# Optimization experiments

Measured on AMD Instinct MI355X. Metric: run time of the kernel, lower is better.

The kernel has to match this reference:

```python
import jax, jax.numpy as jnp
import numpy as np
from jax import lax

B, S, C = 128, 512, 16
V, CV = 50000, 100
E, CE = 100, 30
H = 128        # hidden per direction (hidden_dim=256 // 2)
T = 17         # tagset size
NF = 25        # filters per char-conv
LSTM_IN = E + 3 * NF  # 175


def setup_inputs() -> dict:
    key = jax.random.key(0)
    ks = jax.random.split(key, 25)
    sc = 0.1
    inp = {
        "x": jax.random.randint(ks[0], (B, S), 0, V),
        "char_x": jax.random.randint(ks[1], (B, S, C), 0, CV),
        "tags": jax.random.randint(ks[2], (B, S), 0, T),
        "mask": jnp.ones((B, S), dtype=bool),
        "word_emb": jax.random.normal(ks[3], (V, E), jnp.float32) * sc,
        "char_emb": jax.random.normal(ks[4], (CV, CE), jnp.float32) * sc,
        "conv2_W": jax.random.normal(ks[5], (NF, CE, 2), jnp.float32) * sc,
        "conv2_b": jnp.zeros((NF,), jnp.float32),
        "conv3_W": jax.random.normal(ks[6], (NF, CE, 3), jnp.float32) * sc,
        "conv3_b": jnp.zeros((NF,), jnp.float32),
        "conv4_W": jax.random.normal(ks[7], (NF, CE, 4), jnp.float32) * sc,
        "conv4_b": jnp.zeros((NF,), jnp.float32),
        "W_ih_f": jax.random.normal(ks[8], (4 * H, LSTM_IN), jnp.float32) * sc,
        "W_hh_f": jax.random.normal(ks[9], (4 * H, H), jnp.float32) * sc,
        "b_f": jnp.zeros((4 * H,), jnp.float32),
        "W_ih_b": jax.random.normal(ks[10], (4 * H, LSTM_IN), jnp.float32) * sc,
        "W_hh_b": jax.random.normal(ks[11], (4 * H, H), jnp.float32) * sc,
        "b_b": jnp.zeros((4 * H,), jnp.float32),
        "h2t_W": jax.random.normal(ks[12], (T, 2 * H), jnp.float32) * sc,
        "h2t_b": jnp.zeros((T,), jnp.float32),
        "crf_start": jax.random.normal(ks[13], (T,), jnp.float32) * sc,
        "crf_end": jax.random.normal(ks[14], (T,), jnp.float32) * sc,
        "crf_trans": jax.random.normal(ks[15], (T, T), jnp.float32) * sc,
    }
    return inp


def _char_conv(ce, W, b):
    # ce: [BS, CE, C], W: [O, I, K] -> [BS, O] after relu + max-over-time
    out = lax.conv_general_dilated(ce, W, (1,), 'VALID',
                                   dimension_numbers=('NCH', 'OIH', 'NCH'))
    out = jax.nn.relu(out + b[None, :, None])
    return jnp.max(out, axis=-1)


def _lstm_dir(xs, W_ih, W_hh, b, reverse):
    # xs: [B, S, D] -> hs [B, S, H]; PyTorch gate order i,f,g,o
    xs_t = jnp.swapaxes(xs, 0, 1)  # [S, B, D]
    if reverse:
        xs_t = xs_t[::-1]
    pre = jnp.einsum('sbd,gd->sbg', xs_t, W_ih) + b  # hoist input projection
    h0 = jnp.zeros((xs.shape[0], H), xs.dtype)

    def step(carry, p_t):
        h, c = carry
        g = p_t + h @ W_hh.T
        i = jax.nn.sigmoid(g[:, :H])
        f = jax.nn.sigmoid(g[:, H:2 * H])
        gg = jnp.tanh(g[:, 2 * H:3 * H])
        o = jax.nn.sigmoid(g[:, 3 * H:])
        c = f * c + i * gg
        h = o * jnp.tanh(c)
        return (h, c), h

    _, hs = lax.scan(step, (h0, h0), pre)
    if reverse:
        hs = hs[::-1]
    return jnp.swapaxes(hs, 0, 1)


def _crf_nll(emissions, tags, mask, start, end, trans):
    # emissions [B,S,T]; returns sum over batch of -log p(tags | emissions)
    maskf = mask.astype(emissions.dtype)
    # ---- numerator (gold score) ----
    em_sc = jnp.take_along_axis(emissions, tags[..., None], axis=2)[..., 0]  # [B,S]
    tr_sc = trans[tags[:, :-1], tags[:, 1:]]                                  # [B,S-1]
    last_idx = jnp.sum(mask, axis=1).astype(jnp.int32) - 1
    last_tag = tags[jnp.arange(tags.shape[0]), last_idx]
    score = (start[tags[:, 0]] + em_sc[:, 0]
             + jnp.sum(maskf[:, 1:] * (tr_sc + em_sc[:, 1:]), axis=1)
             + end[last_tag])
    # ---- partition via forward-algorithm scan ----
    em_t = jnp.swapaxes(emissions, 0, 1)  # [S,B,T]
    alpha0 = start[None, :] + em_t[0]     # [B,T]

    def step(alpha, inputs):
        e_t, m_t = inputs  # [B,T], [B]
        new = jax.nn.logsumexp(alpha[:, :, None] + trans[None] + e_t[:, None, :], axis=1)
        alpha = jnp.where(m_t[:, None], new, alpha)
        return alpha, None

    alpha, _ = lax.scan(step, alpha0, (em_t[1:], jnp.swapaxes(mask, 0, 1)[1:]))
    logZ = jax.nn.logsumexp(alpha + end[None, :], axis=1)
    return jnp.sum(logZ - score)


def reference(x, char_x, tags, mask, word_emb, char_emb,
              conv2_W, conv2_b, conv3_W, conv3_b, conv4_W, conv4_b,
              W_ih_f, W_hh_f, b_f, W_ih_b, W_hh_b, b_b,
              h2t_W, h2t_b, crf_start, crf_end, crf_trans):
    # word + char features
    we = word_emb[x]                                     # [B,S,E]
    ce = char_emb[char_x].reshape(B * S, C, CE)          # [BS,C,CE]
    ce = jnp.swapaxes(ce, 1, 2)                          # [BS,CE,C]
    cf = jnp.concatenate([_char_conv(ce, conv2_W, conv2_b),
                          _char_conv(ce, conv3_W, conv3_b),
                          _char_conv(ce, conv4_W, conv4_b)], axis=1)
    cf = cf.reshape(B, S, 3 * NF)
    feats = jnp.concatenate([we, cf], axis=2)            # [B,S,175]
    # BiLSTM
    h_fwd = _lstm_dir(feats, W_ih_f, W_hh_f, b_f, reverse=False)
    h_bwd = _lstm_dir(feats, W_ih_b, W_hh_b, b_b, reverse=True)
    h = jnp.concatenate([h_fwd, h_bwd], axis=2)          # [B,S,2H]
    emissions = jnp.einsum('bsh,th->bst', h, h2t_W) + h2t_b
    # CRF NLL (model returns -crf(...), torchcrf reduction='sum')
    return _crf_nll(emissions, tags, mask, crf_start, crf_end, crf_trans)
```

## Files before the change

kernel.cpp:

```cpp
#include <hip/hip_runtime.h>
#include <hip/hip_bf16.h>

#define B_ 128
#define S_ 512
#define C_ 16
#define E_ 100
#define CE_ 30
#define NF_ 25
#define H_ 128
#define T_ 17
#define LSTM_IN_ 175
#define G4_ 512

typedef __hip_bfloat16 bf16;

__device__ __forceinline__ float bf2f(unsigned short u){
  union { unsigned int i; float f; } v; v.i = ((unsigned int)u) << 16; return v.f;
}
__device__ __forceinline__ float sigm_f(float x){
  float e = __expf(-x);
  return __builtin_amdgcn_rcpf(1.0f + e);
}
__device__ __forceinline__ float tanh_f(float x){
  x = fminf(15.0f, fmaxf(-15.0f, x));
  float e = __expf(-2.0f*x);
  return (1.0f - e) * __builtin_amdgcn_rcpf(1.0f + e);
}

__global__ __launch_bounds__(256) void word_emb_kernel(const int* __restrict__ x,
    const float* __restrict__ wemb, bf16* __restrict__ feats){
  int word = blockIdx.x*2 + (threadIdx.x>>7);
  int e = threadIdx.x & 127;
  if (e < E_) feats[(size_t)word*LSTM_IN_ + e] = __float2bfloat16(wemb[(size_t)x[word]*E_ + e]);
}

template<int KW>
__global__ __launch_bounds__(256) void char_conv_kernel(const int* __restrict__ char_x,
    const float* __restrict__ cemb, const float* __restrict__ W,
    const float* __restrict__ bias, bf16* __restrict__ feats, int out_off){
  int task = blockIdx.x*256 + threadIdx.x;
  int word = task / NF_;
  int fi = task - word*NF_;
  const int* cx = char_x + word*C_;
  float w[KW*CE_];
  #pragma unroll
  for (int i=0;i<KW*CE_;++i) w[i] = W[fi*CE_*KW + i];
  const int NP = C_ - KW + 1;
  float acc[C_ - KW + 1];
  #pragma unroll
  for (int p=0;p<NP;++p) acc[p] = 0.0f;
  #pragma unroll
  for (int c=0;c<C_;++c){
    int ci = cx[c];
    const float* ce = cemb + ci*CE_;
    #pragma unroll
    for (int e=0;e<CE_;++e){
      float v = ce[e];
      #pragma unroll
      for (int dx=0;dx<KW;++dx){
        int p = c - dx;
        if (p >= 0 && p < NP) acc[p] = fmaf(v, w[e*KW+dx], acc[p]);
      }
    }
  }
  float m = acc[0];
  #pragma unroll
  for (int p=1;p<NP;++p) m = fmaxf(m, acc[p]);
  feats[(size_t)word*LSTM_IN_ + out_off + fi] = __float2bfloat16(fmaxf(0.0f, m + bias[fi]));
}

#define BM 128
#define BN 128
#define BK 32
#define LDK 36
__global__ __launch_bounds__(256) void pre_gemm_kernel(const bf16* __restrict__ feats,
    const float* __restrict__ Wf, const float* __restrict__ Wb,
    const float* __restrict__ bf_, const float* __restrict__ bb_,
    bf16* __restrict__ pre){
  __shared__ float As[BM*LDK];
  __shared__ float Bs[BN*LDK];
  int br = blockIdx.x;
  int bc = blockIdx.y;
  int dir = bc >> 2;
  int g0 = (bc & 3) * BN;
  const float* W = dir ? Wb : Wf;
  const float* bias = dir ? bb_ : bf_;
  int tid = threadIdx.x;
  int tr = tid >> 4;
  int tc = tid & 15;
  float acc[8][8];
  #pragma unroll
  for (int i=0;i<8;++i)
    #pragma unroll
    for (int j=0;j<8;++j) acc[i][j] = 0.0f;
  for (int k0 = 0; k0 < LSTM_IN_; k0 += BK){
    for (int l = tid; l < BM*BK; l += 256){
      int r = l >> 5;
      int k = l & 31;
      int kk = k0 + k;
      float av = (kk < LSTM_IN_) ? __bfloat162float(feats[(size_t)(br*BM + r)*LSTM_IN_ + kk]) : 0.0f;
      float bv = (kk < LSTM_IN_) ? W[(size_t)(g0 + r)*LSTM_IN_ + kk] : 0.0f;
      As[r*LDK + k] = av;
      Bs[r*LDK + k] = bv;
    }
    __syncthreads();
    for (int k=0;k<BK;k+=4){
      float4 a4[8], b4[8];
      #pragma unroll
      for (int i=0;i<8;++i) a4[i] = *(const float4*)&As[(tr + 16*i)*LDK + k];
      #pragma unroll
      for (int j=0;j<8;++j) b4[j] = *(const float4*)&Bs[(tc + 16*j)*LDK + k];
      #pragma unroll
      for (int i=0;i<8;++i)
        #pragma unroll
        for (int j=0;j<8;++j){
          acc[i][j] = fmaf(a4[i].x, b4[j].x, acc[i][j]);
          acc[i][j] = fmaf(a4[i].y, b4[j].y, acc[i][j]);
          acc[i][j] = fmaf(a4[i].z, b4[j].z, acc[i][j]);
          acc[i][j] = fmaf(a4[i].w, b4[j].w, acc[i][j]);
        }
    }
    __syncthreads();
  }
  #pragma unroll
  for (int i=0;i<8;++i){
    int word = br*BM + tr + 16*i;
    int b = word >> 9;
    int s = word & 511;
    #pragma unroll
    for (int j=0;j<8;++j){
      int g = g0 + tc + 16*j;
      pre[(size_t)dir*33554432 + (size_t)b*262144 + (size_t)s*512 + g] =
          __float2bfloat16(acc[i][j] + bias[g]);
    }
  }
}

__global__ __launch_bounds__(512) void lstm_kernel(const bf16* __restrict__ pre,
    const float* __restrict__ Whh_f, const float* __restrict__ Whh_b,
    bf16* __restrict__ hs){
  int blk = blockIdx.x;
  int dir = blk & 1;
  int b = blk >> 1;
  int g = threadIdx.x;
  const float* Whh = dir ? Whh_b : Whh_f;
  float w[128];
  {
    const float* Wrow = Whh + g*H_;
    #pragma unroll
    for (int k4=0;k4<32;++k4){
      float4 v = *(const float4*)&Wrow[k4*4];
      w[4*k4+0]=v.x; w[4*k4+1]=v.y; w[4*k4+2]=v.z; w[4*k4+3]=v.w;
    }
  }
  __shared__ __align__(16) float h_lds[H_];
  __shared__ float gates[G4_];
  if (g < H_) h_lds[g] = 0.0f;
  __syncthreads();
  const bf16* preB = pre + ((size_t)dir*B_ + b)*S_*G4_;
  bf16* hsB = hs + ((size_t)dir*B_ + b)*S_*H_;
  float c = 0.0f;
  int sect = g >> 7;
  float nxt = __bfloat162float(preB[(size_t)(dir ? (S_-1) : 0)*G4_ + g]);
  for (int s=0;s<S_;++s){
    int idx = dir ? (S_-1-s) : s;
    float acc = nxt;
    if (s+1 < S_){
      int idx1 = dir ? (S_-2-s) : (s+1);
      nxt = __bfloat162float(preB[(size_t)idx1*G4_ + g]);
    }
    #pragma unroll
    for (int k4=0;k4<32;++k4){
      float4 h4 = *(const float4*)&h_lds[k4*4];
      acc = fmaf(w[4*k4+0], h4.x, acc);
      acc = fmaf(w[4*k4+1], h4.y, acc);
      acc = fmaf(w[4*k4+2], h4.z, acc);
      acc = fmaf(w[4*k4+3], h4.w, acc);
    }
    float a = (sect == 2) ? tanh_f(acc) : sigm_f(acc);
    gates[g] = a;
    __syncthreads();
    if (g < H_){
      float iv = gates[g];
      float fv = gates[g+128];
      float gv = gates[g+256];
      float ov = gates[g+384];
      c = fmaf(fv, c, iv*gv);
      float hn = ov * tanh_f(c);
      h_lds[g] = hn;
      hsB[(size_t)idx*H_ + g] = __float2bfloat16(hn);
    }
    __syncthreads();
  }
}

__global__ __launch_bounds__(256) void emis_kernel(const bf16* __restrict__ hs,
    const float* __restrict__ W, const float* __restrict__ bias, float* __restrict__ em){
  int task = blockIdx.x*256 + threadIdx.x;
  int word = task / T_;
  int t = task - word*T_;
  const ushort4* hf = (const ushort4*)(hs + (size_t)word*H_);
  const ushort4* hb = (const ushort4*)(hs + (size_t)(B_*S_ + word)*H_);
  const float* w0 = W + t*2*H_;
  float acc = bias[t];
  #pragma unroll
  for (int j4=0;j4<32;++j4){
    ushort4 u = hf[j4];
    float4 w4 = *(const float4*)&w0[j4*4];
    acc = fmaf(bf2f(u.x),w4.x,acc); acc = fmaf(bf2f(u.y),w4.y,acc);
    acc = fmaf(bf2f(u.z),w4.z,acc); acc = fmaf(bf2f(u.w),w4.w,acc);
  }
  #pragma unroll
  for (int j4=0;j4<32;++j4){
    ushort4 u = hb[j4];
    float4 w4 = *(const float4*)&w0[H_ + j4*4];
    acc = fmaf(bf2f(u.x),w4.x,acc); acc = fmaf(bf2f(u.y),w4.y,acc);
    acc = fmaf(bf2f(u.z),w4.z,acc); acc = fmaf(bf2f(u.w),w4.w,acc);
  }
  em[(size_t)word*T_ + t] = acc;
}

__global__ __launch_bounds__(256) void score_kernel(const int* __restrict__ tags,
    const float* __restrict__ em, const float* __restrict__ start,
    const float* __restrict__ end_, const float* __restrict__ trans,
    float* __restrict__ score){
  int b = blockIdx.x;
  int tid = threadIdx.x;
  const int* tg = tags + b*S_;
  const float* eb = em + (size_t)b*S_*T_;
  float s = 0.0f;
  for (int t = tid; t < S_; t += 256){
    int cur = tg[t];
    s += eb[(size_t)t*T_ + cur];
    if (t > 0) s += trans[tg[t-1]*T_ + cur];
  }
  if (tid == 0) s += start[tg[0]] + end_[tg[S_-1]];
  __shared__ float red[256];
  red[tid] = s; __syncthreads();
  for (int off=128; off; off>>=1){
    if (tid < off) red[tid] += red[tid+off];
    __syncthreads();
  }
  if (tid == 0) score[b] = red[0];
}

__global__ __launch_bounds__(64) void crf_alpha_kernel(const float* __restrict__ em,
    const float* __restrict__ start, const float* __restrict__ end_,
    const float* __restrict__ trans, float* __restrict__ logZ){
  int b = blockIdx.x;
  int j = threadIdx.x;
  __shared__ float al[T_];
  const float* eb = em + (size_t)b*S_*T_;
  float tcol[T_];
  if (j < T_){
    #pragma unroll
    for (int i=0;i<T_;++i) tcol[i] = trans[i*T_ + j];
    al[j] = start[j] + eb[j];
  }
  __syncthreads();
  float e_cur = (j < T_) ? eb[T_ + j] : 0.0f;
  for (int s=1;s<S_;++s){
    float e_nxt = (j < T_ && s+1 < S_) ? eb[(size_t)(s+1)*T_ + j] : 0.0f;
    float nv = 0.0f;
    if (j < T_){
      float av[T_];
      float m = -1e30f;
      #pragma unroll
      for (int i=0;i<T_;++i){ av[i] = al[i] + tcol[i]; m = fmaxf(m, av[i]); }
      float sum = 0.0f;
      #pragma unroll
      for (int i=0;i<T_;++i) sum += __expf(av[i]-m);
      nv = m + __logf(sum) + e_cur;
    }
    __syncthreads();
    if (j < T_) al[j] = nv;
    __syncthreads();
    e_cur = e_nxt;
  }
  if (j == 0){
    float m = -1e30f;
    float v[T_];
    #pragma unroll
    for (int i=0;i<T_;++i){ v[i] = al[i] + end_[i]; m = fmaxf(m, v[i]); }
    float sum = 0.0f;
    #pragma unroll
    for (int i=0;i<T_;++i) sum += __expf(v[i]-m);
    logZ[b] = m + __logf(sum);
  }
}

__global__ __launch_bounds__(128) void final_kernel(const float* __restrict__ logZ,
    const float* __restrict__ score, float* __restrict__ out){
  int tid = threadIdx.x;
  float v = logZ[tid] - score[tid];
  __shared__ float red[128];
  red[tid] = v; __syncthreads();
  for (int off=64; off; off>>=1){
    if (tid < off) red[tid] += red[tid+off];
    __syncthreads();
  }
  if (tid == 0) out[0] = red[0];
}

extern "C" void kernel_launch(void* const* d_in, const int* in_sizes, int n_in,
                              void* d_out, int out_size, void* d_ws, size_t ws_size,
                              hipStream_t stream) {
  const int*   x       = (const int*)  d_in[0];
  const int*   char_x  = (const int*)  d_in[1];
  const int*   tags    = (const int*)  d_in[2];
  const float* wemb    = (const float*)d_in[4];
  const float* cemb    = (const float*)d_in[5];
  const float* c2W     = (const float*)d_in[6];
  const float* c2b     = (const float*)d_in[7];
  const float* c3W     = (const float*)d_in[8];
  const float* c3b     = (const float*)d_in[9];
  const float* c4W     = (const float*)d_in[10];
  const float* c4b     = (const float*)d_in[11];
  const float* Wih_f   = (const float*)d_in[12];
  const float* Whh_f   = (const float*)d_in[13];
  const float* b_f     = (const float*)d_in[14];
  const float* Wih_b   = (const float*)d_in[15];
  const float* Whh_b   = (const float*)d_in[16];
  const float* b_b     = (const float*)d_in[17];
  const float* h2tW    = (const float*)d_in[18];
  const float* h2tb    = (const float*)d_in[19];
  const float* crf_s   = (const float*)d_in[20];
  const float* crf_e   = (const float*)d_in[21];
  const float* crf_t   = (const float*)d_in[22];
  float* out = (float*)d_out;

  const size_t NEEDED = 190710784ULL;
  if (ws_size < NEEDED) return;
  char* wsb = (char*)d_ws;
  bf16*  feats = (bf16*)(wsb);
  bf16*  pre   = (bf16*)(wsb + 22937600);
  bf16*  hs    = (bf16*)(wsb + 157155328);
  float* em    = (float*)(wsb);
  float* score = (float*)(wsb + 190709760);
  float* logZ  = (float*)(wsb + 190710272);

  word_emb_kernel<<<32768, 256, 0, stream>>>(x, wemb, feats);
  char_conv_kernel<2><<<6400, 256, 0, stream>>>(char_x, cemb, c2W, c2b, feats, E_);
  char_conv_kernel<3><<<6400, 256, 0, stream>>>(char_x, cemb, c3W, c3b, feats, E_ + NF_);
  char_conv_kernel<4><<<6400, 256, 0, stream>>>(char_x, cemb, c4W, c4b, feats, E_ + 2*NF_);
  pre_gemm_kernel<<<dim3(512, 8), 256, 0, stream>>>(feats, Wih_f, Wih_b, b_f, b_b, pre);
  lstm_kernel<<<256, 512, 0, stream>>>(pre, Whh_f, Whh_b, hs);
  emis_kernel<<<4352, 256, 0, stream>>>(hs, h2tW, h2tb, em);
  score_kernel<<<128, 256, 0, stream>>>(tags, em, crf_s, crf_e, crf_t, score);
  crf_alpha_kernel<<<128, 64, 0, stream>>>(em, crf_s, crf_e, crf_t, logZ);
  final_kernel<<<1, 128, 0, stream>>>(logZ, score, out);
}
```

Measured before the change: 1.854 ms.

## Use bf16 MFMA for the input-projection GEMM with K padded to 192

Replaces the scalar fp32 FMA tiled GEMM that computes LSTM input pre-activations with a bf16 MFMA 16x16x32 kernel. Feature rows are padded to 192 columns, with a zero-fill kernel for the padding, and the input weights are packed to bf16 with the same padding by a new kernel, so tiles can be loaded with 16-byte vector loads. The workspace layout is reorganised so feats and hs share a region. The cost is two extra small launches, and the weights are rounded to bf16 before the multiply, which adds precision loss.

```diff
diff --git a/kernel.cpp b/kernel.cpp
--- a/kernel.cpp
+++ b/kernel.cpp
@@ -10,9 +10,12 @@
 #define H_ 128
 #define T_ 17
 #define LSTM_IN_ 175
+#define KP_ 192
 #define G4_ 512
 
 typedef __hip_bfloat16 bf16;
+typedef short bf16x8 __attribute__((ext_vector_type(8)));
+typedef float f32x4 __attribute__((ext_vector_type(4)));
 
 __device__ __forceinline__ float bf2f(unsigned short u){
   union { unsigned int i; float f; } v; v.i = ((unsigned int)u) << 16; return v.f;
@@ -27,11 +30,18 @@
   return (1.0f - e) * __builtin_amdgcn_rcpf(1.0f + e);
 }
 
+__global__ __launch_bounds__(256) void zero_pad_kernel(bf16* __restrict__ feats){
+  int task = blockIdx.x*256 + threadIdx.x;
+  int word = task / 17;
+  int col = LSTM_IN_ + (task - word*17);
+  feats[(size_t)word*KP_ + col] = __float2bfloat16(0.0f);
+}
+
 __global__ __launch_bounds__(256) void word_emb_kernel(const int* __restrict__ x,
     const float* __restrict__ wemb, bf16* __restrict__ feats){
   int word = blockIdx.x*2 + (threadIdx.x>>7);
   int e = threadIdx.x & 127;
-  if (e < E_) feats[(size_t)word*LSTM_IN_ + e] = __float2bfloat16(wemb[(size_t)x[word]*E_ + e]);
+  if (e < E_) feats[(size_t)word*KP_ + e] = __float2bfloat16(wemb[(size_t)x[word]*E_ + e]);
 }
 
 template<int KW>
@@ -66,72 +76,86 @@
   float m = acc[0];
   #pragma unroll
   for (int p=1;p<NP;++p) m = fmaxf(m, acc[p]);
-  feats[(size_t)word*LSTM_IN_ + out_off + fi] = __float2bfloat16(fmaxf(0.0f, m + bias[fi]));
-}
-
-#define BM 128
-#define BN 128
-#define BK 32
-#define LDK 36
-__global__ __launch_bounds__(256) void pre_gemm_kernel(const bf16* __restrict__ feats,
-    const float* __restrict__ Wf, const float* __restrict__ Wb,
-    const float* __restrict__ bf_, const float* __restrict__ bb_,
-    bf16* __restrict__ pre){
-  __shared__ float As[BM*LDK];
-  __shared__ float Bs[BN*LDK];
+  feats[(size_t)word*KP_ + out_off + fi] = __float2bfloat16(fmaxf(0.0f, m + bias[fi]));
+}
+
+__global__ __launch_bounds__(192) void wpack_kernel(const float* __restrict__ Wf,
+    const float* __restrict__ Wb, bf16* __restrict__ wpk){
+  int g = blockIdx.x;
+  int k = threadIdx.x;
+  float v = 0.0f;
+  if (k < LSTM_IN_) v = (g < 512) ? Wf[g*LSTM_IN_ + k] : Wb[(g-512)*LSTM_IN_ + k];
+  wpk[(size_t)g*KP_ + k] = __float2bfloat16(v);
+}
+
+__global__ __launch_bounds__(256) void pre_gemm_mfma(const bf16* __restrict__ feats,
+    const bf16* __restrict__ wpk, const float* __restrict__ bf_,
+    const float* __restrict__ bb_, bf16* __restrict__ pre){
+  __shared__ __align__(16) short As[4096];
+  __shared__ __align__(16) short Bs[4096];
   int br = blockIdx.x;
   int bc = blockIdx.y;
   int dir = bc >> 2;
-  int g0 = (bc & 3) * BN;
-  const float* W = dir ? Wb : Wf;
+  int g0 = (bc & 3) * 128;
   const float* bias = dir ? bb_ : bf_;
   int tid = threadIdx.x;
-  int tr = tid >> 4;
-  int tc = tid & 15;
-  float acc[8][8];
-  #pragma unroll
-  for (int i=0;i<8;++i)
-    #pragma unroll
-    for (int j=0;j<8;++j) acc[i][j] = 0.0f;
-  for (int k0 = 0; k0 < LSTM_IN_; k0 += BK){
-    for (int l = tid; l < BM*BK; l += 256){
-      int r = l >> 5;
-      int k = l & 31;
-      int kk = k0 + k;
-      float av = (kk < LSTM_IN_) ? __bfloat162float(feats[(size_t)(br*BM + r)*LSTM_IN_ + kk]) : 0.0f;
-      float bv = (kk < LSTM_IN_) ? W[(size_t)(g0 + r)*LSTM_IN_ + kk] : 0.0f;
-      As[r*LDK + k] = av;
-      Bs[r*LDK + k] = bv;
-    }
-    __syncthreads();
-    for (int k=0;k<BK;k+=4){
-      float4 a4[8], b4[8];
-      #pragma unroll
-      for (int i=0;i<8;++i) a4[i] = *(const float4*)&As[(tr + 16*i)*LDK + k];
-      #pragma unroll
-      for (int j=0;j<8;++j) b4[j] = *(const float4*)&Bs[(tc + 16*j)*LDK + k];
-      #pragma unroll
-      for (int i=0;i<8;++i)
-        #pragma unroll
-        for (int j=0;j<8;++j){
-          acc[i][j] = fmaf(a4[i].x, b4[j].x, acc[i][j]);
-          acc[i][j] = fmaf(a4[i].y, b4[j].y, acc[i][j]);
-          acc[i][j] = fmaf(a4[i].z, b4[j].z, acc[i][j]);
-          acc[i][j] = fmaf(a4[i].w, b4[j].w, acc[i][j]);
-        }
-    }
-    __syncthreads();
-  }
-  #pragma unroll
-  for (int i=0;i<8;++i){
-    int word = br*BM + tr + 16*i;
-    int b = word >> 9;
-    int s = word & 511;
-    #pragma unroll
-    for (int j=0;j<8;++j){
-      int g = g0 + tc + 16*j;
-      pre[(size_t)dir*33554432 + (size_t)b*262144 + (size_t)s*512 + g] =
-          __float2bfloat16(acc[i][j] + bias[g]);
+  int wave = tid >> 6, lane = tid & 63;
+  int wr = wave >> 1, wc = wave & 1;
+  const bf16* Arow = feats + (size_t)br*128*KP_;
+  const bf16* Brow = wpk + (size_t)(dir*512 + g0)*KP_;
+  f32x4 acc[4][4];
+  #pragma unroll
+  for (int i=0;i<4;++i)
+    #pragma unroll
+    for (int j=0;j<4;++j) acc[i][j] = (f32x4){0.f,0.f,0.f,0.f};
+
+  for (int k0=0; k0<KP_; k0+=32){
+    int4 va[2], vb[2];
+    #pragma unroll
+    for (int hh=0; hh<2; ++hh){
+      int slot = tid + hh*256;
+      int l = slot & 63;
+      int row = ((slot>>6)<<4) + (l & 15);
+      int kb = l >> 4;
+      va[hh] = *(const int4*)(Arow + row*KP_ + k0 + kb*8);
+      vb[hh] = *(const int4*)(Brow + row*KP_ + k0 + kb*8);
+    }
+    __syncthreads();
+    #pragma unroll
+    for (int hh=0; hh<2; ++hh){
+      int slot = tid + hh*256;
+      *(int4*)&As[slot*8] = va[hh];
+      *(int4*)&Bs[slot*8] = vb[hh];
+    }
+    __syncthreads();
+    bf16x8 af[4], bfr[4];
+    #pragma unroll
+    for (int i=0;i<4;++i) af[i]  = *(const bf16x8*)&As[(wr*4+i)*512 + lane*8];
+    #pragma unroll
+    for (int j=0;j<4;++j) bfr[j] = *(const bf16x8*)&Bs[(wc*4+j)*512 + lane*8];
+    #pragma unroll
+    for (int i=0;i<4;++i)
+      #pragma unroll
+      for (int j=0;j<4;++j)
+        acc[i][j] = __builtin_amdgcn_mfma_f32_16x16x32_bf16(af[i], bfr[j], acc[i][j], 0, 0, 0);
+  }
+  int row_l = (lane>>4)*4;
+  int col_l = lane & 15;
+  float bias_v[4];
+  #pragma unroll
+  for (int j=0;j<4;++j) bias_v[j] = bias[g0 + wc*64 + j*16 + col_l];
+  #pragma unroll
+  for (int i=0;i<4;++i){
+    #pragma unroll
+    for (int q=0;q<4;++q){
+      int word = br*128 + wr*64 + i*16 + row_l + q;
+      int bidx = word >> 9, sidx = word & 511;
+      size_t base = ((size_t)(dir*B_ + bidx)*S_ + sidx)*G4_;
+      #pragma unroll
+      for (int j=0;j<4;++j){
+        int g = g0 + wc*64 + j*16 + col_l;
+        pre[base + g] = __float2bfloat16(acc[i][j][q] + bias_v[j]);
+      }
     }
   }
 }
@@ -329,21 +353,24 @@
   const float* crf_t   = (const float*)d_in[22];
   float* out = (float*)d_out;
 
-  const size_t NEEDED = 190710784ULL;
+  const size_t NEEDED = 167773184ULL;
   if (ws_size < NEEDED) return;
   char* wsb = (char*)d_ws;
-  bf16*  feats = (bf16*)(wsb);
-  bf16*  pre   = (bf16*)(wsb + 22937600);
-  bf16*  hs    = (bf16*)(wsb + 157155328);
+  bf16*  pre   = (bf16*)(wsb);
+  bf16*  feats = (bf16*)(wsb + 134217728);
+  bf16*  wpk   = (bf16*)(wsb + 159383552);
+  bf16*  hs    = (bf16*)(wsb + 134217728);
   float* em    = (float*)(wsb);
-  float* score = (float*)(wsb + 190709760);
-  float* logZ  = (float*)(wsb + 190710272);
-
+  float* score = (float*)(wsb + 167772160);
+  float* logZ  = (float*)(wsb + 167772672);
+
+  zero_pad_kernel<<<4352, 256, 0, stream>>>(feats);
   word_emb_kernel<<<32768, 256, 0, stream>>>(x, wemb, feats);
   char_conv_kernel<2><<<6400, 256, 0, stream>>>(char_x, cemb, c2W, c2b, feats, E_);
   char_conv_kernel<3><<<6400, 256, 0, stream>>>(char_x, cemb, c3W, c3b, feats, E_ + NF_);
   char_conv_kernel<4><<<6400, 256, 0, stream>>>(char_x, cemb, c4W, c4b, feats, E_ + 2*NF_);
-  pre_gemm_kernel<<<dim3(512, 8), 256, 0, stream>>>(feats, Wih_f, Wih_b, b_f, b_b, pre);
+  wpack_kernel<<<1024, 192, 0, stream>>>(Wih_f, Wih_b, wpk);
+  pre_gemm_mfma<<<dim3(512, 8), 256, 0, stream>>>(feats, wpk, b_f, b_b, pre);
   lstm_kernel<<<256, 512, 0, stream>>>(pre, Whh_f, Whh_b, hs);
   emis_kernel<<<4352, 256, 0, stream>>>(hs, h2tW, h2tb, em);
   score_kernel<<<128, 256, 0, stream>>>(tags, em, crf_s, crf_e, crf_t, score);
```

Measured after the change: 1.655 ms. 10.7% less time.
